# Kernel optimization log

Measured on AMD Instinct MI355X. Metric: run time of the kernel, lower is better.

Reference implementation:

```python
import jax, jax.numpy as jnp
import numpy as np

L_LAYERS = 6  # weight-tied layer count
ROPE_BASE = 10000.0
LN_EPS = 1e-5


def _ln(x):
    # LayerNorm over last dim, no affine (elementwise_affine=False)
    m = x.mean(-1, keepdims=True)
    v = ((x - m) ** 2).mean(-1, keepdims=True)
    return (x - m) * jax.lax.rsqrt(v + LN_EPS)


def _rope(x):
    # x: (B,H,T,d), d even. Pairs are adjacent (even,odd) indices, cos/sin
    # repeat_interleave(2) pattern, matching the torch implementation.
    d, T = x.shape[-1], x.shape[-2]
    inv_freq = 1.0 / (ROPE_BASE ** (jnp.arange(0, d, 2, dtype=x.dtype) / d))  # (d/2,)
    freqs = jnp.arange(T, dtype=x.dtype)[:, None] * inv_freq[None, :]  # (T, d/2)
    cos, sin = jnp.cos(freqs), jnp.sin(freqs)
    xe, xo = x[..., ::2], x[..., 1::2]
    oe = xe * cos - xo * sin
    oo = xo * cos + xe * sin
    return jnp.stack([oe, oo], axis=-1).reshape(x.shape)


def _attn(Q, K, V):
    # Q,K: (B,H,T,d_head); V: (B,T,D). RoPE + causal softmax, heads averaged.
    d = Q.shape[-1]
    T = Q.shape[-2]
    Qr, Kr = _rope(Q), _rope(K)
    scale = 1.0 / jnp.sqrt(jnp.asarray(d, Q.dtype))
    scores = jnp.einsum('bhtd,bhsd->bhts', Qr, Kr) * scale  # (B,H,T,T)
    causal = jnp.tril(jnp.ones((T, T), dtype=bool))
    scores = jnp.where(causal, scores, -jnp.inf)
    attn = jax.nn.softmax(scores, axis=-1)
    # mean over heads of (attn @ V) == (mean over heads of attn) @ V since V is shared
    attn_mean = attn.mean(axis=1)  # (B,T,T)
    return jnp.einsum('bts,bsd->btd', attn_mean, V)  # (B,T,D)


def setup_inputs() -> dict:
    key = jax.random.key(0)
    ks = jax.random.split(key, 6)
    B, T, D, H, N, V = 2, 256, 256, 4, 32768, 32000
    n = N // H
    std = 0.02
    return {
        'idx': jax.random.randint(ks[0], (B, T), 0, V, dtype=jnp.int32),
        'wte': jax.random.normal(ks[1], (V, D), jnp.float32) * std,
        'encoder': jax.random.normal(ks[2], (N, D), jnp.float32) * std,
        'decoder_x': jax.random.normal(ks[3], (H, D, n), jnp.float32) * std,
        'decoder_y': jax.random.normal(ks[4], (H, D, n), jnp.float32) * std,
        'readout': jax.random.normal(ks[5], (D, V), jnp.float32) * std,
    }


def reference(idx, wte, encoder, decoder_x, decoder_y, readout):
    B, T = idx.shape
    H, D, n = decoder_x.shape
    N = H * n
    v = _ln(wte[idx])  # (B,T,D)
    for _ in range(L_LAYERS):  # weight-tied repeats
        x = jax.nn.relu(jnp.einsum('btd,hdn->bhtn', v, decoder_x))  # (B,H,T,n)
        a = _attn(x, x, v)  # (B,T,D)
        y = jax.nn.relu(jnp.einsum('btd,hdn->bhtn', _ln(a), decoder_y)) * x
        y_flat = y.transpose(0, 2, 1, 3).reshape(B, T, N)  # head-major concat
        v = _ln(v + _ln(y_flat @ encoder))
    return v @ readout  # logits (B,T,vocab)
```

## Files before the change

kernel.cpp:

```cpp
#include <hip/hip_runtime.h>
#include <hip/hip_bf16.h>
#include <math.h>

#define BB   2
#define TT   256
#define DD   256
#define HH   4
#define NN   32768
#define nn   8192
#define VV   32000
#define L_LAYERS 6
#define LN_EPS 1e-5f

#define SKC  8
#define EKC  16

typedef __attribute__((ext_vector_type(8))) short bf16x8;
typedef __attribute__((ext_vector_type(4))) float f32x4;

__device__ __forceinline__ unsigned short f2bf(float f) {
    union { float f; unsigned int u; } v; v.f = f;
    unsigned int r = (v.u + 0x7FFFu + ((v.u >> 16) & 1u)) >> 16;
    return (unsigned short)r;
}
__device__ __forceinline__ float bf2f(unsigned short h) {
    union { unsigned int u; float f; } v; v.u = ((unsigned int)h) << 16;
    return v.f;
}
__device__ __forceinline__ bf16x8 ld_frag(const unsigned short* p) {
    union { bf16x8 v; uint2 u[2]; } r;
    r.u[0] = *(const uint2*)(p);
    r.u[1] = *(const uint2*)(p + 4);
    return r.v;
}

__device__ __forceinline__ float block_sum(float v) {
    __shared__ float sh[4];
    #pragma unroll
    for (int o = 32; o > 0; o >>= 1) v += __shfl_down(v, o, 64);
    __syncthreads();
    if ((threadIdx.x & 63) == 0) sh[threadIdx.x >> 6] = v;
    __syncthreads();
    return sh[0] + sh[1] + sh[2] + sh[3];
}
__device__ __forceinline__ float block_max(float v) {
    __shared__ float sh[4];
    #pragma unroll
    for (int o = 32; o > 0; o >>= 1) v = fmaxf(v, __shfl_down(v, o, 64));
    __syncthreads();
    if ((threadIdx.x & 63) == 0) sh[threadIdx.x >> 6] = v;
    __syncthreads();
    return fmaxf(fmaxf(sh[0], sh[1]), fmaxf(sh[2], sh[3]));
}
__device__ __forceinline__ float ln_val(float x) {
    float m = block_sum(x) * (1.0f / 256.0f);
    float d = x - m;
    float var = block_sum(d * d) * (1.0f / 256.0f);
    return d * rsqrtf(var + LN_EPS);
}

__global__ __launch_bounds__(256) void embed_ln_k(const int* __restrict__ idx,
                                                  const float* __restrict__ wte,
                                                  float* __restrict__ v,
                                                  unsigned short* __restrict__ vb) {
    int row = blockIdx.x;
    int tok = idx[row];
    float x = wte[(size_t)tok * DD + threadIdx.x];
    float o = ln_val(x);
    size_t i = (size_t)row * DD + threadIdx.x;
    v[i] = o;
    vb[i] = f2bf(o);
}

__global__ __launch_bounds__(256) void ln_rows_k(const float* __restrict__ in,
                                                 unsigned short* __restrict__ ob) {
    size_t i = (size_t)blockIdx.x * DD + threadIdx.x;
    ob[i] = f2bf(ln_val(in[i]));
}

__global__ __launch_bounds__(256) void add_ln_ln_k(float* __restrict__ v,
                                                   const float* __restrict__ yencp,
                                                   unsigned short* __restrict__ vb) {
    size_t i = (size_t)blockIdx.x * DD + threadIdx.x;
    float ysum = 0.0f;
    #pragma unroll
    for (int kc = 0; kc < EKC; kc++)
        ysum += yencp[(size_t)kc * (BB * TT * DD) + i];
    float t1 = ln_val(ysum);
    float w = v[i] + t1;
    float o = ln_val(w);
    v[i] = o;
    vb[i] = f2bf(o);
}

__global__ __launch_bounds__(256) void tconv_k(const float* __restrict__ src,
                                               unsigned short* __restrict__ dst,
                                               int R, int C, long sstride, long dstride) {
    src += (size_t)blockIdx.z * sstride;
    dst += (size_t)blockIdx.z * dstride;
    __shared__ unsigned short tile[64][66];
    int c0 = blockIdx.x * 64, r0 = blockIdx.y * 64;
    int c = threadIdx.x & 63, q = threadIdx.x >> 6;
    #pragma unroll
    for (int i = 0; i < 16; i++) {
        int r = q + i * 4;
        tile[r][c] = f2bf(src[(size_t)(r0 + r) * C + c0 + c]);
    }
    __syncthreads();
    #pragma unroll
    for (int i = 0; i < 16; i++) {
        int r = q + i * 4;
        dst[(size_t)(c0 + r) * R + r0 + c] = tile[c][r];
    }
}

__device__ __forceinline__ void bt_mainloop64(const unsigned short* Ap, long lda,
                                              const unsigned short* Bp, long ldb,
                                              int ksteps,
                                              unsigned short (*As)[68],
                                              unsigned short (*Bs)[68],
                                              f32x4 (&acc)[4][4]) {
    int tid = threadIdx.x;
    int ra = tid >> 1, pa = (tid & 1) * 32;
    int lane = tid & 63, w = tid >> 6;
    int rowoff = (w >> 1) * 64, coloff = (w & 1) * 64;
    int fr = lane & 15, fq = (lane >> 4) * 8;
    const unsigned short* ga = Ap + (size_t)ra * lda + pa;
    const unsigned short* gb = Bp + (size_t)ra * ldb + pa;
    uint4 a0 = *(const uint4*)ga,        a1 = *(const uint4*)(ga + 8);
    uint4 a2 = *(const uint4*)(ga + 16), a3 = *(const uint4*)(ga + 24);
    uint4 b0 = *(const uint4*)gb,        b1 = *(const uint4*)(gb + 8);
    uint4 b2 = *(const uint4*)(gb + 16), b3 = *(const uint4*)(gb + 24);
    for (int k = 0; k < ksteps; k++) {
        __syncthreads();
        uint2* da = (uint2*)&As[ra][pa];
        da[0] = make_uint2(a0.x, a0.y); da[1] = make_uint2(a0.z, a0.w);
        da[2] = make_uint2(a1.x, a1.y); da[3] = make_uint2(a1.z, a1.w);
        da[4] = make_uint2(a2.x, a2.y); da[5] = make_uint2(a2.z, a2.w);
        da[6] = make_uint2(a3.x, a3.y); da[7] = make_uint2(a3.z, a3.w);
        uint2* db = (uint2*)&Bs[ra][pa];
        db[0] = make_uint2(b0.x, b0.y); db[1] = make_uint2(b0.z, b0.w);
        db[2] = make_uint2(b1.x, b1.y); db[3] = make_uint2(b1.z, b1.w);
        db[4] = make_uint2(b2.x, b2.y); db[5] = make_uint2(b2.z, b2.w);
        db[6] = make_uint2(b3.x, b3.y); db[7] = make_uint2(b3.z, b3.w);
        if (k + 1 < ksteps) {
            ga += 64; gb += 64;
            a0 = *(const uint4*)ga;        a1 = *(const uint4*)(ga + 8);
            a2 = *(const uint4*)(ga + 16); a3 = *(const uint4*)(ga + 24);
            b0 = *(const uint4*)gb;        b1 = *(const uint4*)(gb + 8);
            b2 = *(const uint4*)(gb + 16); b3 = *(const uint4*)(gb + 24);
        }
        __syncthreads();
        #pragma unroll
        for (int ks = 0; ks < 2; ks++) {
            bf16x8 af[4], bfv[4];
            #pragma unroll
            for (int mi = 0; mi < 4; mi++)
                af[mi] = ld_frag(&As[rowoff + mi * 16 + fr][ks * 32 + fq]);
            #pragma unroll
            for (int nj = 0; nj < 4; nj++)
                bfv[nj] = ld_frag(&Bs[coloff + nj * 16 + fr][ks * 32 + fq]);
            #pragma unroll
            for (int mi = 0; mi < 4; mi++)
                #pragma unroll
                for (int nj = 0; nj < 4; nj++)
                    acc[mi][nj] = __builtin_amdgcn_mfma_f32_16x16x32_bf16(af[mi], bfv[nj], acc[mi][nj], 0, 0, 0);
        }
    }
}

__global__ __launch_bounds__(256) void gemm_head_bt(const unsigned short* __restrict__ A,
                                                    const unsigned short* __restrict__ Wt,
                                                    unsigned short* __restrict__ Cx,
                                                    const unsigned short* __restrict__ mulx,
                                                    unsigned short* __restrict__ Cy,
                                                    int mode) {
    int h = blockIdx.z;
    int n0 = blockIdx.x * 128, m0 = blockIdx.y * 128;
    __shared__ __attribute__((aligned(16))) unsigned short smem[17408];
    unsigned short (*As)[68] = (unsigned short (*)[68])smem;
    unsigned short (*Bs)[68] = (unsigned short (*)[68])(smem + 8704);
    f32x4 acc[4][4] = {};
    bt_mainloop64(A + (size_t)m0 * DD, DD,
                  Wt + (size_t)h * nn * DD + (size_t)n0 * DD, DD, 4, As, Bs, acc);
    __syncthreads();

    int tid = threadIdx.x, lane = tid & 63, w = tid >> 6;
    int rowoff = (w >> 1) * 64, coloff = (w & 1) * 64;
    int r4 = (lane >> 4) * 4, cc = lane & 15;
    unsigned short (*Cs)[128] = (unsigned short (*)[128])smem;
    #pragma unroll
    for (int mi = 0; mi < 4; mi++)
        #pragma unroll
        for (int nj = 0; nj < 4; nj++)
            #pragma unroll
            for (int rr = 0; rr < 4; rr++)
                Cs[rowoff + mi * 16 + r4 + rr][coloff + nj * 16 + cc] =
                    f2bf(fmaxf(acc[mi][nj][rr], 0.0f));
    __syncthreads();

    int colc = (tid & 15) * 8;
    #pragma unroll
    for (int j = 0; j < 8; j++) {
        int row = (tid >> 4) + j * 16;
        int m = m0 + row;
        int b = m >> 8, t = m & 255;
        union { uint4 u; unsigned short s[8]; } ch;
        ch.u = *(const uint4*)&Cs[row][colc];
        size_t bhtn = (((size_t)(b * HH + h)) * TT + t) * (size_t)nn + n0 + colc;
        if (mode == 0) {
            *(uint4*)(Cx + bhtn) = ch.u;
            union { uint4 u; unsigned short s[8]; } ro;
            float tf = (float)t;
            int pbase = ((n0 + colc) >> 1);
            #pragma unroll
            for (int k2 = 0; k2 < 4; k2++) {
                int p = pbase + k2;
                float inv = __expf(-(float)p * (9.210340371976184f / 4096.0f));
                float ang = tf * inv;
                float s = __sinf(ang), c = __cosf(ang);
                float xe = bf2f(ch.s[2 * k2]), xo = bf2f(ch.s[2 * k2 + 1]);
                ro.s[2 * k2]     = f2bf(xe * c - xo * s);
                ro.s[2 * k2 + 1] = f2bf(xo * c + xe * s);
            }
            *(uint4*)(Cy + bhtn) = ro.u;
        } else {
            union { uint4 u; unsigned short s[8]; } mx, oy;
            mx.u = *(const uint4*)(mulx + bhtn);
            #pragma unroll
            for (int k2 = 0; k2 < 8; k2++)
                oy.s[k2] = f2bf(bf2f(ch.s[k2]) * bf2f(mx.s[k2]));
            *(uint4*)(Cy + ((size_t)(b * TT + t)) * NN + (size_t)h * nn + n0 + colc) = oy.u;
        }
    }
}

__global__ __launch_bounds__(256) void scores_bt(const unsigned short* __restrict__ xrb,
                                                 float* __restrict__ scp) {
    int zh = blockIdx.z, kc = blockIdx.y, tile = blockIdx.x;
    int t0 = (tile >= 1) ? 128 : 0;
    int s0 = (tile == 2) ? 128 : 0;
    const unsigned short* Xz = xrb + (size_t)zh * TT * nn + (size_t)kc * (nn / SKC);
    __shared__ __attribute__((aligned(16))) unsigned short As[128][68], Bs[128][68];
    f32x4 acc[4][4] = {};
    bt_mainloop64(Xz + (size_t)t0 * nn, nn, Xz + (size_t)s0 * nn, nn, (nn / SKC) / 64,
                  As, Bs, acc);
    const float scale = 0.011048543456039805f;
    int tid = threadIdx.x, lane = tid & 63, w = tid >> 6;
    int rowoff = (w >> 1) * 64, coloff = (w & 1) * 64;
    int r4 = (lane >> 4) * 4, cc = lane & 15;
    float* dst = scp + ((size_t)(zh * 3 + tile) * SKC + kc) * 16384;
    #pragma unroll
    for (int mi = 0; mi < 4; mi++)
        #pragma unroll
        for (int nj = 0; nj < 4; nj++)
            #pragma unroll
            for (int rr = 0; rr < 4; rr++) {
                int r = rowoff + mi * 16 + r4 + rr;
                int c = coloff + nj * 16 + cc;
                dst[r * 128 + c] = acc[mi][nj][rr] * scale;
            }
}

__global__ __launch_bounds__(256) void gemm_enc_bt(const unsigned short* __restrict__ A,
                                                   const unsigned short* __restrict__ Bt,
                                                   float* __restrict__ yencp) {
    int n0 = blockIdx.x * 128, m0 = blockIdx.y * 128;
    int kc = blockIdx.z;
    long kbase = (long)kc * (NN / EKC);
    __shared__ __attribute__((aligned(16))) unsigned short As[128][68], Bs[128][68];
    f32x4 acc[4][4] = {};
    bt_mainloop64(A + (size_t)m0 * NN + kbase, NN,
                  Bt + (size_t)n0 * NN + kbase, NN, (NN / EKC) / 64, As, Bs, acc);
    int tid = threadIdx.x, lane = tid & 63, w = tid >> 6;
    int rowoff = (w >> 1) * 64, coloff = (w & 1) * 64;
    int r4 = (lane >> 4) * 4, cc = lane & 15;
    float* C = yencp + (size_t)kc * (BB * TT * DD);
    #pragma unroll
    for (int mi = 0; mi < 4; mi++)
        #pragma unroll
        for (int nj = 0; nj < 4; nj++)
            #pragma unroll
            for (int rr = 0; rr < 4; rr++) {
                int row = m0 + rowoff + mi * 16 + r4 + rr;
                int col = n0 + coloff + nj * 16 + cc;
                C[(size_t)row * DD + col] = acc[mi][nj][rr];
            }
}

__global__ __launch_bounds__(256) void gemm_ro_bt(const unsigned short* __restrict__ A,
                                                  const unsigned short* __restrict__ Wt,
                                                  float* __restrict__ out) {
    int n0 = blockIdx.x * 128, m0 = blockIdx.y * 128;
    __shared__ __attribute__((aligned(16))) unsigned short As[128][68], Bs[128][68];
    f32x4 acc[4][4] = {};
    bt_mainloop64(A + (size_t)m0 * DD, DD, Wt + (size_t)n0 * DD, DD, 4, As, Bs, acc);
    int tid = threadIdx.x, lane = tid & 63, w = tid >> 6;
    int rowoff = (w >> 1) * 64, coloff = (w & 1) * 64;
    int r4 = (lane >> 4) * 4, cc = lane & 15;
    #pragma unroll
    for (int mi = 0; mi < 4; mi++)
        #pragma unroll
        for (int nj = 0; nj < 4; nj++)
            #pragma unroll
            for (int rr = 0; rr < 4; rr++) {
                int m = m0 + rowoff + mi * 16 + r4 + rr;
                int col = n0 + coloff + nj * 16 + cc;
                out[(size_t)m * VV + col] = acc[mi][nj][rr];
            }
}

__global__ __launch_bounds__(256) void softmax_mean_k(const float* __restrict__ scp,
                                                      float* __restrict__ am) {
    int bt = blockIdx.x;
    int b = bt >> 8, t = bt & 255;
    int s = threadIdx.x;
    int tr = t & 127, scol = s & 127;
    int tileid = (t >= 128) ? ((s >= 128) ? 2 : 1) : 0;
    float acc = 0.0f;
    for (int h = 0; h < HH; h++) {
        int zh = b * HH + h;
        float val = -1e30f;
        if (s <= t) {
            const float* p = scp + ((size_t)(zh * 3 + tileid) * SKC) * 16384
                           + tr * 128 + scol;
            float v0 = 0.0f;
            #pragma unroll
            for (int kc = 0; kc < SKC; kc++) v0 += p[(size_t)kc * 16384];
            val = v0;
        }
        float mx = block_max(val);
        float e = (s <= t) ? expf(val - mx) : 0.0f;
        float sum = block_sum(e);
        acc += e / sum;
    }
    am[((size_t)b * TT + t) * TT + s] = acc * 0.25f;
}

__global__ __launch_bounds__(256) void gemm_nn_k(const float* __restrict__ A,
                                                 const float* __restrict__ B,
                                                 float* __restrict__ C,
                                                 int M, int N, int K,
                                                 long lda, long ldb, long ldc,
                                                 long sAz, long sBz, long sCz) {
    int batch = blockIdx.z;
    A += (size_t)batch * sAz;
    B += (size_t)batch * sBz;
    C += (size_t)batch * sCz;
    int m0 = blockIdx.y * 64, n0 = blockIdx.x * 64;
    __shared__ float As[16][68];
    __shared__ float Bs[16][64];
    int tid = threadIdx.x;
    int tx = tid & 15, ty = tid >> 4;
    int ar = tid >> 2, ac = (tid & 3) * 4;
    int br = tid >> 4, bc = (tid & 15) * 4;
    float acc[4][4] = {};
    for (int k0 = 0; k0 < K; k0 += 16) {
        float4 av = *(const float4*)(A + (size_t)(m0 + ar) * lda + k0 + ac);
        float4 bv = *(const float4*)(B + (size_t)(k0 + br) * ldb + n0 + bc);
        As[ac + 0][ar] = av.x; As[ac + 1][ar] = av.y;
        As[ac + 2][ar] = av.z; As[ac + 3][ar] = av.w;
        *(float4*)&Bs[br][bc] = bv;
        __syncthreads();
        #pragma unroll
        for (int k = 0; k < 16; k++) {
            float4 a4 = *(const float4*)&As[k][ty * 4];
            float4 b4 = *(const float4*)&Bs[k][tx * 4];
            float aa[4] = {a4.x, a4.y, a4.z, a4.w};
            float bb[4] = {b4.x, b4.y, b4.z, b4.w};
            #pragma unroll
            for (int i = 0; i < 4; i++)
                #pragma unroll
                for (int j = 0; j < 4; j++)
                    acc[i][j] = fmaf(aa[i], bb[j], acc[i][j]);
        }
        __syncthreads();
    }
    #pragma unroll
    for (int i = 0; i < 4; i++) {
        int m = m0 + ty * 4 + i;
        #pragma unroll
        for (int j = 0; j < 4; j++) {
            int col = n0 + tx * 4 + j;
            C[(size_t)m * ldc + col] = acc[i][j];
        }
    }
}

extern "C" void kernel_launch(void* const* d_in, const int* in_sizes, int n_in,
                              void* d_out, int out_size, void* d_ws, size_t ws_size,
                              hipStream_t stream) {
    const int*   idx  = (const int*)d_in[0];
    const float* wte  = (const float*)d_in[1];
    const float* enc  = (const float*)d_in[2];
    const float* Wx   = (const float*)d_in[3];
    const float* Wy   = (const float*)d_in[4];
    const float* Wro  = (const float*)d_in[5];
    float* out = (float*)d_out;

    float* ws   = (float*)d_ws;
    float* v    = ws;
    float* am   = v   + 131072;
    float* a    = am  + 131072;
    float* red  = a   + 131072;
    unsigned short* sbase = (unsigned short*)(red + 3145728);
    unsigned short* vb   = sbase;
    unsigned short* lAb  = vb   + 131072;
    unsigned short* xb   = lAb  + 131072;
    unsigned short* xrb  = xb   + 16777216;
    unsigned short* WxT  = xrb  + 16777216;
    unsigned short* WyT  = WxT  + 8388608;
    unsigned short* encT = WyT  + 8388608;
    unsigned short* ybf  = xrb;
    unsigned short* WroT = xb;
    float* yencp = red;

    tconv_k<<<dim3(nn / 64, DD / 64, HH), 256, 0, stream>>>(Wx, WxT, DD, nn,
        (long)DD * nn, (long)nn * DD);
    tconv_k<<<dim3(DD / 64, NN / 64, 1), 256, 0, stream>>>(enc, encT, NN, DD, 0L, 0L);
    tconv_k<<<dim3(nn / 64, DD / 64, HH), 256, 0, stream>>>(Wy, WyT, DD, nn,
        (long)DD * nn, (long)nn * DD);

    embed_ln_k<<<BB * TT, 256, 0, stream>>>(idx, wte, v, vb);

    for (int l = 0; l < L_LAYERS; l++) {
        gemm_head_bt<<<dim3(nn / 128, (BB * TT) / 128, HH), 256, 0, stream>>>(
            vb, WxT, xb, nullptr, xrb, 0);

        scores_bt<<<dim3(3, SKC, BB * HH), 256, 0, stream>>>(xrb, red);

        softmax_mean_k<<<BB * TT, 256, 0, stream>>>(red, am);

        gemm_nn_k<<<dim3(DD / 64, TT / 64, BB), 256, 0, stream>>>(
            am, v, a, TT, DD, TT,
            (long)TT, (long)DD, (long)DD,
            (long)TT * TT, (long)TT * DD, (long)TT * DD);

        ln_rows_k<<<BB * TT, 256, 0, stream>>>(a, lAb);

        gemm_head_bt<<<dim3(nn / 128, (BB * TT) / 128, HH), 256, 0, stream>>>(
            lAb, WyT, nullptr, xb, ybf, 1);

        gemm_enc_bt<<<dim3(2, 4, EKC), 256, 0, stream>>>(ybf, encT, yencp);

        add_ln_ln_k<<<BB * TT, 256, 0, stream>>>(v, yencp, vb);
    }

    tconv_k<<<dim3(VV / 64, DD / 64, 1), 256, 0, stream>>>(Wro, WroT, DD, VV, 0L, 0L);

    gemm_ro_bt<<<dim3(VV / 128, (BB * TT) / 128, 1), 256, 0, stream>>>(vb, WroT, out);
}
```

Baseline: 1.004 ms.

## Drop unrotated x buffer by inverse-RoPE recompute, fuse per-head softmax reductions

The first head GEMM no longer writes the unrotated relu output x. The second head GEMM rebuilds x from the RoPE-rotated buffer by applying the inverse rotation, which removes a 32 MB write and its separate read. The softmax-mean kernel now reduces all four heads together with wave shuffles and only two barriers instead of eight block reductions. The encoder GEMM split-K factor doubles, and its partials move into the freed xrb region. The cost is extra sin/cos/exp work and some bf16 round-trip error from rotating and then unrotating x.

```diff
diff --git a/kernel.cpp b/kernel.cpp
--- a/kernel.cpp
+++ b/kernel.cpp
@@ -13,7 +13,7 @@
 #define LN_EPS 1e-5f
 
 #define SKC  8
-#define EKC  16
+#define EKC  32
 
 typedef __attribute__((ext_vector_type(8))) short bf16x8;
 typedef __attribute__((ext_vector_type(4))) float f32x4;
@@ -171,8 +171,7 @@
 
 __global__ __launch_bounds__(256) void gemm_head_bt(const unsigned short* __restrict__ A,
                                                     const unsigned short* __restrict__ Wt,
-                                                    unsigned short* __restrict__ Cx,
-                                                    const unsigned short* __restrict__ mulx,
+                                                    const unsigned short* __restrict__ xr,
                                                     unsigned short* __restrict__ Cy,
                                                     int mode) {
     int h = blockIdx.z;
@@ -208,11 +207,10 @@
         union { uint4 u; unsigned short s[8]; } ch;
         ch.u = *(const uint4*)&Cs[row][colc];
         size_t bhtn = (((size_t)(b * HH + h)) * TT + t) * (size_t)nn + n0 + colc;
+        float tf = (float)t;
+        int pbase = ((n0 + colc) >> 1);
         if (mode == 0) {
-            *(uint4*)(Cx + bhtn) = ch.u;
             union { uint4 u; unsigned short s[8]; } ro;
-            float tf = (float)t;
-            int pbase = ((n0 + colc) >> 1);
             #pragma unroll
             for (int k2 = 0; k2 < 4; k2++) {
                 int p = pbase + k2;
@@ -225,11 +223,20 @@
             }
             *(uint4*)(Cy + bhtn) = ro.u;
         } else {
-            union { uint4 u; unsigned short s[8]; } mx, oy;
-            mx.u = *(const uint4*)(mulx + bhtn);
-            #pragma unroll
-            for (int k2 = 0; k2 < 8; k2++)
-                oy.s[k2] = f2bf(bf2f(ch.s[k2]) * bf2f(mx.s[k2]));
+            union { uint4 u; unsigned short s[8]; } xu, oy;
+            xu.u = *(const uint4*)(xr + bhtn);
+            #pragma unroll
+            for (int k2 = 0; k2 < 4; k2++) {
+                int p = pbase + k2;
+                float inv = __expf(-(float)p * (9.210340371976184f / 4096.0f));
+                float ang = tf * inv;
+                float s = __sinf(ang), c = __cosf(ang);
+                float oe = bf2f(xu.s[2 * k2]), oo = bf2f(xu.s[2 * k2 + 1]);
+                float xe = oe * c + oo * s;
+                float xo = oo * c - oe * s;
+                oy.s[2 * k2]     = f2bf(bf2f(ch.s[2 * k2])     * xe);
+                oy.s[2 * k2 + 1] = f2bf(bf2f(ch.s[2 * k2 + 1]) * xo);
+            }
             *(uint4*)(Cy + ((size_t)(b * TT + t)) * NN + (size_t)h * nn + n0 + colc) = oy.u;
         }
     }
@@ -315,24 +322,61 @@
     int bt = blockIdx.x;
     int b = bt >> 8, t = bt & 255;
     int s = threadIdx.x;
+    int lane = s & 63, wid = s >> 6;
     int tr = t & 127, scol = s & 127;
     int tileid = (t >= 128) ? ((s >= 128) ? 2 : 1) : 0;
-    float acc = 0.0f;
+    float val[HH];
+    #pragma unroll
     for (int h = 0; h < HH; h++) {
         int zh = b * HH + h;
-        float val = -1e30f;
+        float v0 = -1e30f;
         if (s <= t) {
             const float* p = scp + ((size_t)(zh * 3 + tileid) * SKC) * 16384
                            + tr * 128 + scol;
-            float v0 = 0.0f;
+            v0 = 0.0f;
             #pragma unroll
             for (int kc = 0; kc < SKC; kc++) v0 += p[(size_t)kc * 16384];
-            val = v0;
-        }
-        float mx = block_max(val);
-        float e = (s <= t) ? expf(val - mx) : 0.0f;
-        float sum = block_sum(e);
-        acc += e / sum;
+        }
+        val[h] = v0;
+    }
+    __shared__ float smx[4][4], ssm[4][4];
+    float m0 = val[0], m1 = val[1], m2 = val[2], m3 = val[3];
+    #pragma unroll
+    for (int o = 32; o > 0; o >>= 1) {
+        m0 = fmaxf(m0, __shfl_down(m0, o, 64));
+        m1 = fmaxf(m1, __shfl_down(m1, o, 64));
+        m2 = fmaxf(m2, __shfl_down(m2, o, 64));
+        m3 = fmaxf(m3, __shfl_down(m3, o, 64));
+    }
+    if (lane == 0) { smx[wid][0] = m0; smx[wid][1] = m1; smx[wid][2] = m2; smx[wid][3] = m3; }
+    __syncthreads();
+    float e[HH];
+    float e0, e1, e2, e3;
+    {
+        float mh0 = fmaxf(fmaxf(smx[0][0], smx[1][0]), fmaxf(smx[2][0], smx[3][0]));
+        float mh1 = fmaxf(fmaxf(smx[0][1], smx[1][1]), fmaxf(smx[2][1], smx[3][1]));
+        float mh2 = fmaxf(fmaxf(smx[0][2], smx[1][2]), fmaxf(smx[2][2], smx[3][2]));
+        float mh3 = fmaxf(fmaxf(smx[0][3], smx[1][3]), fmaxf(smx[2][3], smx[3][3]));
+        bool act = (s <= t);
+        e[0] = e0 = act ? expf(val[0] - mh0) : 0.0f;
+        e[1] = e1 = act ? expf(val[1] - mh1) : 0.0f;
+        e[2] = e2 = act ? expf(val[2] - mh2) : 0.0f;
+        e[3] = e3 = act ? expf(val[3] - mh3) : 0.0f;
+    }
+    #pragma unroll
+    for (int o = 32; o > 0; o >>= 1) {
+        e0 += __shfl_down(e0, o, 64);
+        e1 += __shfl_down(e1, o, 64);
+        e2 += __shfl_down(e2, o, 64);
+        e3 += __shfl_down(e3, o, 64);
+    }
+    if (lane == 0) { ssm[wid][0] = e0; ssm[wid][1] = e1; ssm[wid][2] = e2; ssm[wid][3] = e3; }
+    __syncthreads();
+    float acc = 0.0f;
+    #pragma unroll
+    for (int h = 0; h < HH; h++) {
+        float sum = ssm[0][h] + ssm[1][h] + ssm[2][h] + ssm[3][h];
+        acc += e[h] / sum;
     }
     am[((size_t)b * TT + t) * TT + s] = acc * 0.25f;
 }
@@ -404,16 +448,16 @@
     float* a    = am  + 131072;
     float* red  = a   + 131072;
     unsigned short* sbase = (unsigned short*)(red + 3145728);
-    unsigned short* vb   = sbase;
-    unsigned short* lAb  = vb   + 131072;
-    unsigned short* xb   = lAb  + 131072;
-    unsigned short* xrb  = xb   + 16777216;
-    unsigned short* WxT  = xrb  + 16777216;
-    unsigned short* WyT  = WxT  + 8388608;
-    unsigned short* encT = WyT  + 8388608;
-    unsigned short* ybf  = xrb;
-    unsigned short* WroT = xb;
-    float* yencp = red;
+    unsigned short* vb    = sbase;
+    unsigned short* lAb   = vb    + 131072;
+    unsigned short* ybreg = lAb   + 131072;
+    unsigned short* xrb   = ybreg + 16777216;
+    unsigned short* WxT   = xrb   + 16777216;
+    unsigned short* WyT   = WxT   + 8388608;
+    unsigned short* encT  = WyT   + 8388608;
+    unsigned short* ybf   = ybreg;
+    unsigned short* WroT  = ybreg;
+    float* yencp = (float*)xrb;
 
     tconv_k<<<dim3(nn / 64, DD / 64, HH), 256, 0, stream>>>(Wx, WxT, DD, nn,
         (long)DD * nn, (long)nn * DD);
@@ -425,7 +469,7 @@
 
     for (int l = 0; l < L_LAYERS; l++) {
         gemm_head_bt<<<dim3(nn / 128, (BB * TT) / 128, HH), 256, 0, stream>>>(
-            vb, WxT, xb, nullptr, xrb, 0);
+            vb, WxT, nullptr, xrb, 0);
 
         scores_bt<<<dim3(3, SKC, BB * HH), 256, 0, stream>>>(xrb, red);
 
@@ -439,7 +483,7 @@
         ln_rows_k<<<BB * TT, 256, 0, stream>>>(a, lAb);
 
         gemm_head_bt<<<dim3(nn / 128, (BB * TT) / 128, HH), 256, 0, stream>>>(
-            lAb, WyT, nullptr, xb, ybf, 1);
+            lAb, WyT, xrb, ybf, 1);
 
         gemm_enc_bt<<<dim3(2, 4, EKC), 256, 0, stream>>>(ybf, encT, yencp);
 
```

Result: faster. 937.3 us (-6.7%).
